# Performance work log

Hardware: AMD Instinct MI355X
Metric: run time of the kernel (lower is better)

The kernel has to match this reference:

```python
import jax, jax.numpy as jnp
import numpy as np

NEG_SLOPE = 0.01
LN_EPS = 1e-5

def _layer_norm(h, g, b):
    mu = jnp.mean(h, axis=-1, keepdims=True)
    var = jnp.mean(jnp.square(h - mu), axis=-1, keepdims=True)
    return (h - mu) * jax.lax.rsqrt(var + LN_EPS) * g + b

def _mlp(h, Wa, ba, g, be, Wb, bb):
    h = h @ Wa + ba
    h = jnp.where(h >= 0, h, NEG_SLOPE * h)  # LeakyReLU
    h = _layer_norm(h, g, be)
    return h @ Wb + bb

def setup_inputs() -> dict:
    N, E = 50000, 800000
    DN, DE, DG, DO = 128, 64, 32, 128
    key = jax.random.key(0)
    ks = jax.random.split(key, 16)
    def lin(k, fan_in, fan_out):
        lim = 1.0 / np.sqrt(fan_in)
        k1, k2 = jax.random.split(k)
        W = jax.random.uniform(k1, (fan_in, fan_out), jnp.float32, -lim, lim)
        b = jax.random.uniform(k2, (fan_out,), jnp.float32, -lim, lim)
        return W, b
    W1a, b1a = lin(ks[0], DN + DE + DG, DO)
    W1b, b1b = lin(ks[1], DO, DO)
    W2a, b2a = lin(ks[2], DN + DO, DO)
    W2b, b2b = lin(ks[3], DO, DO)
    return {
        "x": jax.random.normal(ks[4], (N, DN), jnp.float32),
        "edge_index": jax.random.randint(ks[5], (2, E), 0, N, jnp.int32),
        "edge_attr": jax.random.normal(ks[6], (E, DE), jnp.float32),
        "u": jax.random.normal(ks[7], (DG,), jnp.float32),
        "batch": jnp.zeros((N,), jnp.int32),
        "W1a": W1a, "b1a": b1a,
        "g1": jnp.ones((DO,), jnp.float32), "be1": jnp.zeros((DO,), jnp.float32),
        "W1b": W1b, "b1b": b1b,
        "W2a": W2a, "b2a": b2a,
        "g2": jnp.ones((DO,), jnp.float32), "be2": jnp.zeros((DO,), jnp.float32),
        "W2b": W2b, "b2b": b2b,
    }

def reference(x, edge_index, edge_attr, u, batch,
              W1a, b1a, g1, be1, W1b, b1b,
              W2a, b2a, g2, be2, W2b, b2b):
    src, dest = edge_index[0], edge_index[1]
    E = edge_attr.shape[0]
    N = x.shape[0]
    # gather + concat: [E, DN+DE+DG]
    h = jnp.concatenate([x[src], edge_attr,
                         jnp.broadcast_to(u[None, :], (E, u.shape[0]))], axis=1)
    h = _mlp(h, W1a, b1a, g1, be1, W1b, b1b)
    # scatter_mean by dest
    sums = jax.ops.segment_sum(h, dest, num_segments=N)
    cnt = jax.ops.segment_sum(jnp.ones((E,), h.dtype), dest, num_segments=N)
    agg = sums / jnp.maximum(cnt, 1.0)[:, None]
    return _mlp(jnp.concatenate([x, agg], axis=1), W2a, b2a, g2, be2, W2b, b2b)
```

## Files before the change

kernel.cpp:

```cpp
#include <hip/hip_runtime.h>
#include <hip/hip_fp16.h>
#include <hip/hip_bf16.h>

constexpr int DN = 128, DE = 64, DG = 32, DO = 128;
constexpr float NEG_SLOPE = 0.01f;
constexpr float LN_EPS = 1e-5f;

constexpr int EPB = 128;
constexpr int NB  = 64;
constexpr int T_LD = 136;
constexpr int H_LD = 132;

typedef __attribute__((ext_vector_type(8))) short bf16x8;
typedef __attribute__((ext_vector_type(4))) float f32x4;

__device__ inline unsigned short f2bf(float f) {
    unsigned u = __builtin_bit_cast(unsigned, f);
    u += 0x7FFFu + ((u >> 16) & 1u);
    return (unsigned short)(u >> 16);
}

__device__ inline bf16x8 pk8(float4 p, float4 q) {
    bf16x8 r;
    r[0] = (short)f2bf(p.x); r[1] = (short)f2bf(p.y);
    r[2] = (short)f2bf(p.z); r[3] = (short)f2bf(p.w);
    r[4] = (short)f2bf(q.x); r[5] = (short)f2bf(q.y);
    r[6] = (short)f2bf(q.z); r[7] = (short)f2bf(q.w);
    return r;
}

__global__ void wprep_kernel(const float* __restrict__ W1a,
                             const float* __restrict__ W1b,
                             const float* __restrict__ W2a,
                             const float* __restrict__ W2b,
                             const float* __restrict__ b1a,
                             const float* __restrict__ b1b,
                             const float* __restrict__ u,
                             unsigned short* __restrict__ tab,
                             float* __restrict__ bc,
                             float* __restrict__ b1ap) {
    int idx = blockIdx.x * 256 + threadIdx.x;
    if (idx >= 18 * 512 + 256) return;
    if (idx >= 18 * 512 + 128) {
        int n = idx - (18 * 512 + 128);
        float s = b1a[n];
        for (int k = 0; k < DG; ++k) s += u[k] * W1a[(long)(192 + k) * DO + n];
        b1ap[n] = s;
        return;
    }
    if (idx >= 18 * 512) {
        int n = idx - 18 * 512;
        float s = 0.f;
        for (int j = 0; j < DO; ++j) s += b1b[j] * W2a[(long)(DN + j) * DO + n];
        bc[n] = s;
        return;
    }
    int slabset = idx >> 9;
    int rem = idx & 511;
    int nt = rem >> 6, lane = rem & 63;
    int quad = lane >> 4, l15 = lane & 15;
    int n = nt * 16 + l15;
    union { ushort4 u4[2]; unsigned short s[8]; } o;
    if (slabset < 6) {
        int k0 = slabset * 32 + quad * 8;
#pragma unroll
        for (int j = 0; j < 8; ++j) o.s[j] = f2bf(W1a[(long)(k0 + j) * DO + n]);
    } else if (slabset < 10) {
        int k0 = (slabset - 6) * 32 + quad * 8;
#pragma unroll
        for (int j = 0; j < 8; ++j) o.s[j] = f2bf(W2a[(long)(k0 + j) * DO + n]);
    } else if (slabset < 14) {
        int k0 = (slabset - 10) * 32 + quad * 8;
        float s[8] = {0.f, 0.f, 0.f, 0.f, 0.f, 0.f, 0.f, 0.f};
        for (int j2 = 0; j2 < DO; ++j2) {
            float wa = W2a[(long)(DN + j2) * DO + n];
#pragma unroll
            for (int j = 0; j < 8; ++j) s[j] += W1b[(long)(k0 + j) * DO + j2] * wa;
        }
#pragma unroll
        for (int j = 0; j < 8; ++j) o.s[j] = f2bf(s[j]);
    } else {
        int k0 = (slabset - 14) * 32 + quad * 8;
#pragma unroll
        for (int j = 0; j < 8; ++j) o.s[j] = f2bf(W2b[(long)(k0 + j) * DO + n]);
    }
    *(ushort4*)&tab[(long)idx * 8]     = o.u4[0];
    *(ushort4*)&tab[(long)idx * 8 + 4] = o.u4[1];
}

__global__ void hist_kernel(const int* __restrict__ edge_index,
                            int* __restrict__ counts, int E) {
    int e = blockIdx.x * 256 + threadIdx.x;
    if (e < E) atomicAdd(&counts[edge_index[E + e]], 1);
}

__global__ __launch_bounds__(1024) void scan1_kernel(
    const int* __restrict__ counts, int* __restrict__ offsets,
    int* __restrict__ partials, int N) {
    __shared__ int s_ws[16];
    const int tid = threadIdx.x, lane = tid & 63, wv = tid >> 6;
    int i = blockIdx.x * 1024 + tid;
    int v = (i < N) ? counts[i] : 0;
    int s = v;
#pragma unroll
    for (int off = 1; off < 64; off <<= 1) {
        int t = __shfl_up(s, off, 64);
        if (lane >= off) s += t;
    }
    if (lane == 63) s_ws[wv] = s;
    __syncthreads();
    if (tid < 16) {
        int w = s_ws[tid];
#pragma unroll
        for (int off = 1; off < 16; off <<= 1) {
            int t = __shfl_up(w, off, 16);
            if (tid >= off) w += t;
        }
        s_ws[tid] = w;
    }
    __syncthreads();
    int wbase = wv ? s_ws[wv - 1] : 0;
    if (i < N) offsets[i] = wbase + s - v;
    if (tid == 0) partials[blockIdx.x] = s_ws[15];
}

__global__ void scan2_kernel(int* __restrict__ partials, int P) {
    const int t = threadIdx.x;
    int carry = 0;
    for (int base = 0; base < P; base += 64) {
        int idx = base + t;
        int v = (idx < P) ? partials[idx] : 0;
        int s = v;
#pragma unroll
        for (int off = 1; off < 64; off <<= 1) {
            int w = __shfl_up(s, off, 64);
            if (t >= off) s += w;
        }
        if (idx < P) partials[idx] = carry + s - v;
        carry += __shfl(s, 63, 64);
    }
}

__global__ __launch_bounds__(1024) void scan3_kernel(
    int* __restrict__ offsets, const int* __restrict__ partials,
    int* __restrict__ cursor, int N, int E) {
    int i = blockIdx.x * 1024 + threadIdx.x;
    if (i < N) {
        int o = offsets[i] + partials[blockIdx.x];
        offsets[i] = o; cursor[i] = o;
    }
    if (i == 0) offsets[N] = E;
}

__global__ void scatter_kernel(const int* __restrict__ edge_index,
                               int* __restrict__ cursor,
                               int2* __restrict__ sorted, int E) {
    int e = blockIdx.x * 256 + threadIdx.x;
    if (e < E) {
        int d = edge_index[E + e];
        int pos = atomicAdd(&cursor[d], 1);
        sorted[pos] = make_int2(e, d);
    }
}

__global__ __launch_bounds__(256) void edge_kernel(
    const float* __restrict__ x, const int* __restrict__ edge_index,
    const float* __restrict__ edge_attr,
    const int2* __restrict__ sorted, const unsigned short* __restrict__ tab,
    const float* __restrict__ b1ap, const float* __restrict__ g1,
    const float* __restrict__ be1,
    float* __restrict__ sums, int E)
{
    __shared__ int s_src[EPB], s_eid[EPB], s_dst[EPB];
    __shared__ alignas(16) __half s_h[EPB * H_LD];

    const int tid = threadIdx.x, lane = tid & 63, wave = tid >> 6;
    const int l15 = lane & 15, quad = lane >> 4;
    const int ebase = blockIdx.x * EPB;
    const int evalid = min(EPB, E - ebase);

    if (tid < EPB) {
        bool v = tid < evalid;
        int2 ed = v ? sorted[ebase + tid] : make_int2(0, 0);
        s_eid[tid] = ed.x;
        s_dst[tid] = ed.y;
        s_src[tid] = edge_index[ed.x];
    }
    __syncthreads();

    const int r0 = wave * 32 + l15, r1 = r0 + 16;
    const long xs0 = (long)s_src[r0] * DN;
    const long xs1 = (long)s_src[r1] * DN;
    const long er0 = (long)s_eid[r0] * DE;
    const long er1 = (long)s_eid[r1] * DE;
    const bf16x8* tW1a = (const bf16x8*)tab;
    const int kq = quad * 8;

    f32x4 acc[2][8];
#pragma unroll
    for (int mt = 0; mt < 2; ++mt)
#pragma unroll
        for (int nt = 0; nt < 8; ++nt) acc[mt][nt] = (f32x4){0.f, 0.f, 0.f, 0.f};

#pragma unroll
    for (int ks = 0; ks < 6; ++ks) {
        float4 p0, q0, p1, q1;
        if (ks < 4) {
            const float* b0 = &x[xs0 + ks * 32 + kq];
            const float* b1 = &x[xs1 + ks * 32 + kq];
            p0 = *(const float4*)b0; q0 = *(const float4*)(b0 + 4);
            p1 = *(const float4*)b1; q1 = *(const float4*)(b1 + 4);
        } else {
            int c = ks * 32 - DN + kq;
            const float* b0 = &edge_attr[er0 + c];
            const float* b1 = &edge_attr[er1 + c];
            p0 = *(const float4*)b0; q0 = *(const float4*)(b0 + 4);
            p1 = *(const float4*)b1; q1 = *(const float4*)(b1 + 4);
        }
        bf16x8 a0 = pk8(p0, q0);
        bf16x8 a1 = pk8(p1, q1);
#pragma unroll
        for (int nt = 0; nt < 8; ++nt) {
            bf16x8 b = tW1a[(ks * 8 + nt) * 64 + lane];
            acc[0][nt] = __builtin_amdgcn_mfma_f32_16x16x32_bf16(a0, b, acc[0][nt], 0, 0, 0);
            acc[1][nt] = __builtin_amdgcn_mfma_f32_16x16x32_bf16(a1, b, acc[1][nt], 0, 0, 0);
        }
    }

    float ba[8], gg[8], bb[8];
#pragma unroll
    for (int nt = 0; nt < 8; ++nt) {
        int col = nt * 16 + l15;
        ba[nt] = b1ap[col]; gg[nt] = g1[col]; bb[nt] = be1[col];
    }
#pragma unroll
    for (int mt = 0; mt < 2; ++mt) {
#pragma unroll
        for (int r = 0; r < 4; ++r) {
            float v[8];
            float s = 0.f, q = 0.f;
#pragma unroll
            for (int nt = 0; nt < 8; ++nt) {
                float t = acc[mt][nt][r] + ba[nt];
                t = (t >= 0.f) ? t : NEG_SLOPE * t;
                v[nt] = t; s += t; q += t * t;
            }
#pragma unroll
            for (int off = 1; off < 16; off <<= 1) {
                s += __shfl_xor(s, off, 64);
                q += __shfl_xor(q, off, 64);
            }
            float mu  = s * (1.f / DO);
            float var = q * (1.f / DO) - mu * mu;
            float rs  = rsqrtf(var + LN_EPS);
            int lrow = wave * 32 + mt * 16 + quad * 4 + r;
#pragma unroll
            for (int nt = 0; nt < 8; ++nt) {
                float h  = (v[nt] - mu) * rs * gg[nt] + bb[nt];
                float hp = __shfl_xor(h, 1, 64);
                if ((l15 & 1) == 0) {
                    *(__half2*)&s_h[lrow * H_LD + nt * 16 + l15] =
                        __halves2half2(__float2half_rn(h), __float2half_rn(hp));
                }
            }
        }
    }
    __syncthreads();

    {
        const int d2 = lane * 2;
        int e0 = wave * 32, e1 = min(e0 + 32, evalid);
        if (e0 < e1) {
            float a0 = 0.f, a1 = 0.f;
            int cur = s_dst[e0];
            if (e1 - e0 == 32) {
#pragma unroll
                for (int k = 0; k < 32; ++k) {
                    int e = e0 + k;
                    int dd = s_dst[e];
                    if (dd != cur) {
                        unsafeAtomicAdd(&sums[(long)cur * DO + d2], a0);
                        unsafeAtomicAdd(&sums[(long)cur * DO + d2 + 1], a1);
                        a0 = a1 = 0.f; cur = dd;
                    }
                    float2 hv = __half22float2(*(const __half2*)&s_h[e * H_LD + d2]);
                    a0 += hv.x; a1 += hv.y;
                }
            } else {
                for (int e = e0; e < e1; ++e) {
                    int dd = s_dst[e];
                    if (dd != cur) {
                        unsafeAtomicAdd(&sums[(long)cur * DO + d2], a0);
                        unsafeAtomicAdd(&sums[(long)cur * DO + d2 + 1], a1);
                        a0 = a1 = 0.f; cur = dd;
                    }
                    float2 hv = __half22float2(*(const __half2*)&s_h[e * H_LD + d2]);
                    a0 += hv.x; a1 += hv.y;
                }
            }
            unsafeAtomicAdd(&sums[(long)cur * DO + d2], a0);
            unsafeAtomicAdd(&sums[(long)cur * DO + d2 + 1], a1);
        }
    }
}

__global__ __launch_bounds__(256) void node_kernel(
    const float* __restrict__ x, const float* __restrict__ sums,
    const int* __restrict__ offsets, const unsigned short* __restrict__ tab,
    const float* __restrict__ bc,
    const float* __restrict__ b2a, const float* __restrict__ g2,
    const float* __restrict__ be2, const float* __restrict__ b2b,
    float* __restrict__ out, int N)
{
    __shared__ unsigned short s_t[4][16 * T_LD];

    const int tid = threadIdx.x, lane = tid & 63, wave = tid >> 6;
    const int l15 = lane & 15, quad = lane >> 4;
    const int nbase = blockIdx.x * NB;

    const bf16x8* tW2aT = (const bf16x8*)tab + 6 * 512;
    const bf16x8* tWc   = (const bf16x8*)tab + 10 * 512;
    const bf16x8* tW2b  = (const bf16x8*)tab + 14 * 512;

    const int nodeA = min(nbase + wave * 16 + l15, N - 1);
    const int cntA  = offsets[nodeA + 1] - offsets[nodeA];
    const float invc = 1.f / fmaxf((float)cntA, 1.f);
    const int kq = quad * 8;

    f32x4 acc[8];

#pragma unroll
    for (int nt = 0; nt < 8; ++nt) acc[nt] = (f32x4){0.f, 0.f, 0.f, 0.f};
#pragma unroll
    for (int ks = 0; ks < 8; ++ks) {
        bf16x8 a;
        if (ks < 4) {
            const float* b0 = &x[(long)nodeA * DN + ks * 32 + kq];
            a = pk8(*(const float4*)b0, *(const float4*)(b0 + 4));
        } else {
            const float* sp = &sums[(long)nodeA * DO + (ks - 4) * 32 + kq];
            float4 p = *(const float4*)sp;
            float4 q = *(const float4*)(sp + 4);
            p.x *= invc; p.y *= invc; p.z *= invc; p.w *= invc;
            q.x *= invc; q.y *= invc; q.z *= invc; q.w *= invc;
            a = pk8(p, q);
        }
        const bf16x8* tB = (ks < 4) ? tW2aT : tWc;
        const int kk = (ks < 4) ? ks : ks - 4;
#pragma unroll
        for (int nt = 0; nt < 8; ++nt) {
            bf16x8 b = tB[(kk * 8 + nt) * 64 + lane];
            acc[nt] = __builtin_amdgcn_mfma_f32_16x16x32_bf16(a, b, acc[nt], 0, 0, 0);
        }
    }
    {
        float ba[8], gg[8], bb[8], bcv[8];
#pragma unroll
        for (int nt = 0; nt < 8; ++nt) {
            int col = nt * 16 + l15;
            ba[nt] = b2a[col]; gg[nt] = g2[col]; bb[nt] = be2[col]; bcv[nt] = bc[col];
        }
#pragma unroll
        for (int reg = 0; reg < 4; ++reg) {
            int nodeC = nbase + wave * 16 + quad * 4 + reg;
            int cc = (nodeC < N) ? (offsets[nodeC + 1] - offsets[nodeC]) : 0;
            float cf = (cc > 0) ? 1.f : 0.f;
            float v[8];
            float s = 0.f, q = 0.f;
#pragma unroll
            for (int nt = 0; nt < 8; ++nt) {
                float t = acc[nt][reg] + ba[nt] + cf * bcv[nt];
                t = (t >= 0.f) ? t : NEG_SLOPE * t;
                v[nt] = t; s += t; q += t * t;
            }
#pragma unroll
            for (int off = 1; off < 16; off <<= 1) {
                s += __shfl_xor(s, off, 64);
                q += __shfl_xor(q, off, 64);
            }
            float mu  = s * (1.f / DO);
            float var = q * (1.f / DO) - mu * mu;
            float rs  = rsqrtf(var + LN_EPS);
            int lrow = quad * 4 + reg;
#pragma unroll
            for (int nt = 0; nt < 8; ++nt) {
                float h = (v[nt] - mu) * rs * gg[nt] + bb[nt];
                s_t[wave][lrow * T_LD + nt * 16 + l15] = f2bf(h);
            }
        }
    }

#pragma unroll
    for (int nt = 0; nt < 8; ++nt) acc[nt] = (f32x4){0.f, 0.f, 0.f, 0.f};
#pragma unroll
    for (int ks = 0; ks < 4; ++ks) {
        bf16x8 a = *(const bf16x8*)&s_t[wave][l15 * T_LD + ks * 32 + kq];
#pragma unroll
        for (int nt = 0; nt < 8; ++nt) {
            bf16x8 b = tW2b[(ks * 8 + nt) * 64 + lane];
            acc[nt] = __builtin_amdgcn_mfma_f32_16x16x32_bf16(a, b, acc[nt], 0, 0, 0);
        }
    }
    {
#pragma unroll
        for (int reg = 0; reg < 4; ++reg) {
            int nodeC = nbase + wave * 16 + quad * 4 + reg;
            if (nodeC < N) {
                long base = (long)nodeC * DO;
#pragma unroll
                for (int nt = 0; nt < 8; ++nt)
                    out[base + nt * 16 + l15] = acc[nt][reg] + b2b[nt * 16 + l15];
            }
        }
    }
}

extern "C" void kernel_launch(void* const* d_in, const int* in_sizes, int n_in,
                              void* d_out, int out_size, void* d_ws, size_t ws_size,
                              hipStream_t stream)
{
    const float* x          = (const float*)d_in[0];
    const int*   edge_index = (const int*)d_in[1];
    const float* edge_attr  = (const float*)d_in[2];
    const float* u          = (const float*)d_in[3];
    const float* W1a = (const float*)d_in[5];
    const float* b1a = (const float*)d_in[6];
    const float* g1  = (const float*)d_in[7];
    const float* be1 = (const float*)d_in[8];
    const float* W1b = (const float*)d_in[9];
    const float* b1b = (const float*)d_in[10];
    const float* W2a = (const float*)d_in[11];
    const float* b2a = (const float*)d_in[12];
    const float* g2  = (const float*)d_in[13];
    const float* be2 = (const float*)d_in[14];
    const float* W2b = (const float*)d_in[15];
    const float* b2b = (const float*)d_in[16];

    const int N = in_sizes[0] / DN;
    const int E = in_sizes[2] / DE;
    float* out  = (float*)d_out;

    char* p = (char*)d_ws;
    int2* sorted = (int2*)p;                   p += (size_t)E * sizeof(int2);
    unsigned short* tab = (unsigned short*)p;  p += (size_t)18 * 512 * 8 * sizeof(unsigned short);
    float* bc = (float*)p;                     p += 128 * sizeof(float);
    float* b1ap = (float*)p;                   p += 128 * sizeof(float);
    int* counts = (int*)p;                     p += (size_t)N * sizeof(int);
    int* offsets = (int*)p;                    p += (size_t)(N + 1) * sizeof(int);
    p = (char*)(((uintptr_t)p + 15) & ~(uintptr_t)15);
    int* partials = (int*)p;                   p += 64 * sizeof(int);
    int* cursor = (int*)p;                     p += (size_t)N * sizeof(int);
    float* sums = (float*)d_out;

    (void)hipMemsetAsync(counts, 0, (size_t)N * sizeof(int), stream);
    (void)hipMemsetAsync(d_out, 0, (size_t)N * DO * sizeof(float), stream);

    wprep_kernel<<<(18 * 512 + 256 + 255) / 256, 256, 0, stream>>>(
        W1a, W1b, W2a, W2b, b1a, b1b, u, tab, bc, b1ap);

    const int P = (N + 1023) / 1024;
    hist_kernel<<<(E + 255) / 256, 256, 0, stream>>>(edge_index, counts, E);
    scan1_kernel<<<P, 1024, 0, stream>>>(counts, offsets, partials, N);
    scan2_kernel<<<1, 64, 0, stream>>>(partials, P);
    scan3_kernel<<<P, 1024, 0, stream>>>(offsets, partials, cursor, N, E);
    scatter_kernel<<<(E + 255) / 256, 256, 0, stream>>>(edge_index, cursor, sorted, E);

    const int eblocks = (E + EPB - 1) / EPB;
    edge_kernel<<<eblocks, 256, 0, stream>>>(
        x, edge_index, edge_attr, sorted, tab, b1ap, g1, be1, sums, E);

    const int nblocks = (N + NB - 1) / NB;
    node_kernel<<<nblocks, 256, 0, stream>>>(
        x, sums, offsets, tab, bc, b2a, g2, be2, b2b, out, N);
}
```

Measured before the change: 728.7 us.

## Pre-convert x to bf16, merge scan passes, shrink node blocks, drop edge syncs

Adds a prep kernel that converts x to bf16 once, so the edge kernel's random gathers of source rows move half the bytes and skip per-edge conversion. The second scan pass is folded into the third, which removes one launch. The node kernel now runs one wave per block with 16 nodes. The edge kernel's block-wide barriers are removed by having each wave load only its own edge indices. The cost is an extra full pass over x and a risk of races if any shared data is still read across waves without a barrier.

```diff
diff --git a/kernel.cpp b/kernel.cpp
--- a/kernel.cpp
+++ b/kernel.cpp
@@ -7,7 +7,7 @@
 constexpr float LN_EPS = 1e-5f;
 
 constexpr int EPB = 128;
-constexpr int NB  = 64;
+constexpr int NB  = 16;
 constexpr int T_LD = 136;
 constexpr int H_LD = 132;
 
@@ -88,6 +88,16 @@
     *(ushort4*)&tab[(long)idx * 8 + 4] = o.u4[1];
 }
 
+__global__ void xprep_kernel(const float* __restrict__ x,
+                             unsigned short* __restrict__ xb, int total8) {
+    int i = blockIdx.x * 256 + threadIdx.x;
+    if (i < total8) {
+        const float4* p = (const float4*)x + (long)i * 2;
+        bf16x8 r = pk8(p[0], p[1]);
+        *(bf16x8*)&xb[(long)i * 8] = r;
+    }
+}
+
 __global__ void hist_kernel(const int* __restrict__ edge_index,
                             int* __restrict__ counts, int E) {
     int e = blockIdx.x * 256 + threadIdx.x;
@@ -124,29 +134,25 @@
     if (tid == 0) partials[blockIdx.x] = s_ws[15];
 }
 
-__global__ void scan2_kernel(int* __restrict__ partials, int P) {
-    const int t = threadIdx.x;
-    int carry = 0;
-    for (int base = 0; base < P; base += 64) {
-        int idx = base + t;
-        int v = (idx < P) ? partials[idx] : 0;
-        int s = v;
-#pragma unroll
-        for (int off = 1; off < 64; off <<= 1) {
-            int w = __shfl_up(s, off, 64);
-            if (t >= off) s += w;
-        }
-        if (idx < P) partials[idx] = carry + s - v;
-        carry += __shfl(s, 63, 64);
-    }
-}
-
 __global__ __launch_bounds__(1024) void scan3_kernel(
     int* __restrict__ offsets, const int* __restrict__ partials,
-    int* __restrict__ cursor, int N, int E) {
-    int i = blockIdx.x * 1024 + threadIdx.x;
+    int* __restrict__ cursor, int N, int E, int P) {
+    __shared__ int s_base;
+    const int tid = threadIdx.x;
+    if (tid < 64) {
+        int v = (tid < P) ? partials[tid] : 0;
+        int s = v;
+#pragma unroll
+        for (int off = 1; off < 64; off <<= 1) {
+            int t = __shfl_up(s, off, 64);
+            if (tid >= off) s += t;
+        }
+        if (tid == (int)blockIdx.x) s_base = s - v;
+    }
+    __syncthreads();
+    int i = blockIdx.x * 1024 + tid;
     if (i < N) {
-        int o = offsets[i] + partials[blockIdx.x];
+        int o = offsets[i] + s_base;
         offsets[i] = o; cursor[i] = o;
     }
     if (i == 0) offsets[N] = E;
@@ -164,7 +170,7 @@
 }
 
 __global__ __launch_bounds__(256) void edge_kernel(
-    const float* __restrict__ x, const int* __restrict__ edge_index,
+    const unsigned short* __restrict__ xb, const int* __restrict__ edge_index,
     const float* __restrict__ edge_attr,
     const int2* __restrict__ sorted, const unsigned short* __restrict__ tab,
     const float* __restrict__ b1ap, const float* __restrict__ g1,
@@ -179,14 +185,14 @@
     const int ebase = blockIdx.x * EPB;
     const int evalid = min(EPB, E - ebase);
 
-    if (tid < EPB) {
-        bool v = tid < evalid;
-        int2 ed = v ? sorted[ebase + tid] : make_int2(0, 0);
-        s_eid[tid] = ed.x;
-        s_dst[tid] = ed.y;
-        s_src[tid] = edge_index[ed.x];
-    }
-    __syncthreads();
+    if (lane < 32) {
+        int r = wave * 32 + lane;
+        bool v = r < evalid;
+        int2 ed = v ? sorted[ebase + r] : make_int2(0, 0);
+        s_eid[r] = ed.x;
+        s_dst[r] = ed.y;
+        s_src[r] = edge_index[ed.x];
+    }
 
     const int r0 = wave * 32 + l15, r1 = r0 + 16;
     const long xs0 = (long)s_src[r0] * DN;
@@ -204,21 +210,17 @@
 
 #pragma unroll
     for (int ks = 0; ks < 6; ++ks) {
-        float4 p0, q0, p1, q1;
+        bf16x8 a0, a1;
         if (ks < 4) {
-            const float* b0 = &x[xs0 + ks * 32 + kq];
-            const float* b1 = &x[xs1 + ks * 32 + kq];
-            p0 = *(const float4*)b0; q0 = *(const float4*)(b0 + 4);
-            p1 = *(const float4*)b1; q1 = *(const float4*)(b1 + 4);
+            a0 = *(const bf16x8*)&xb[xs0 + ks * 32 + kq];
+            a1 = *(const bf16x8*)&xb[xs1 + ks * 32 + kq];
         } else {
             int c = ks * 32 - DN + kq;
             const float* b0 = &edge_attr[er0 + c];
             const float* b1 = &edge_attr[er1 + c];
-            p0 = *(const float4*)b0; q0 = *(const float4*)(b0 + 4);
-            p1 = *(const float4*)b1; q1 = *(const float4*)(b1 + 4);
-        }
-        bf16x8 a0 = pk8(p0, q0);
-        bf16x8 a1 = pk8(p1, q1);
+            a0 = pk8(*(const float4*)b0, *(const float4*)(b0 + 4));
+            a1 = pk8(*(const float4*)b1, *(const float4*)(b1 + 4));
+        }
 #pragma unroll
         for (int nt = 0; nt < 8; ++nt) {
             bf16x8 b = tW1a[(ks * 8 + nt) * 64 + lane];
@@ -265,7 +267,6 @@
             }
         }
     }
-    __syncthreads();
 
     {
         const int d2 = lane * 2;
@@ -304,17 +305,17 @@
     }
 }
 
-__global__ __launch_bounds__(256) void node_kernel(
-    const float* __restrict__ x, const float* __restrict__ sums,
+__global__ __launch_bounds__(64) void node_kernel(
+    const unsigned short* __restrict__ xb, const float* __restrict__ sums,
     const int* __restrict__ offsets, const unsigned short* __restrict__ tab,
     const float* __restrict__ bc,
     const float* __restrict__ b2a, const float* __restrict__ g2,
     const float* __restrict__ be2, const float* __restrict__ b2b,
     float* __restrict__ out, int N)
 {
-    __shared__ unsigned short s_t[4][16 * T_LD];
-
-    const int tid = threadIdx.x, lane = tid & 63, wave = tid >> 6;
+    __shared__ unsigned short s_t[16 * T_LD];
+
+    const int lane = threadIdx.x;
     const int l15 = lane & 15, quad = lane >> 4;
     const int nbase = blockIdx.x * NB;
 
@@ -322,7 +323,7 @@
     const bf16x8* tWc   = (const bf16x8*)tab + 10 * 512;
     const bf16x8* tW2b  = (const bf16x8*)tab + 14 * 512;
 
-    const int nodeA = min(nbase + wave * 16 + l15, N - 1);
+    const int nodeA = min(nbase + l15, N - 1);
     const int cntA  = offsets[nodeA + 1] - offsets[nodeA];
     const float invc = 1.f / fmaxf((float)cntA, 1.f);
     const int kq = quad * 8;
@@ -335,8 +336,7 @@
     for (int ks = 0; ks < 8; ++ks) {
         bf16x8 a;
         if (ks < 4) {
-            const float* b0 = &x[(long)nodeA * DN + ks * 32 + kq];
-            a = pk8(*(const float4*)b0, *(const float4*)(b0 + 4));
+            a = *(const bf16x8*)&xb[(long)nodeA * DN + ks * 32 + kq];
         } else {
             const float* sp = &sums[(long)nodeA * DO + (ks - 4) * 32 + kq];
             float4 p = *(const float4*)sp;
@@ -362,7 +362,7 @@
         }
 #pragma unroll
         for (int reg = 0; reg < 4; ++reg) {
-            int nodeC = nbase + wave * 16 + quad * 4 + reg;
+            int nodeC = nbase + quad * 4 + reg;
             int cc = (nodeC < N) ? (offsets[nodeC + 1] - offsets[nodeC]) : 0;
             float cf = (cc > 0) ? 1.f : 0.f;
             float v[8];
@@ -385,7 +385,7 @@
 #pragma unroll
             for (int nt = 0; nt < 8; ++nt) {
                 float h = (v[nt] - mu) * rs * gg[nt] + bb[nt];
-                s_t[wave][lrow * T_LD + nt * 16 + l15] = f2bf(h);
+                s_t[lrow * T_LD + nt * 16 + l15] = f2bf(h);
             }
         }
     }
@@ -394,7 +394,7 @@
     for (int nt = 0; nt < 8; ++nt) acc[nt] = (f32x4){0.f, 0.f, 0.f, 0.f};
 #pragma unroll
     for (int ks = 0; ks < 4; ++ks) {
-        bf16x8 a = *(const bf16x8*)&s_t[wave][l15 * T_LD + ks * 32 + kq];
+        bf16x8 a = *(const bf16x8*)&s_t[l15 * T_LD + ks * 32 + kq];
 #pragma unroll
         for (int nt = 0; nt < 8; ++nt) {
             bf16x8 b = tW2b[(ks * 8 + nt) * 64 + lane];
@@ -404,7 +404,7 @@
     {
 #pragma unroll
         for (int reg = 0; reg < 4; ++reg) {
-            int nodeC = nbase + wave * 16 + quad * 4 + reg;
+            int nodeC = nbase + quad * 4 + reg;
             if (nodeC < N) {
                 long base = (long)nodeC * DO;
 #pragma unroll
@@ -442,6 +442,7 @@
 
     char* p = (char*)d_ws;
     int2* sorted = (int2*)p;                   p += (size_t)E * sizeof(int2);
+    unsigned short* xb = (unsigned short*)p;   p += (size_t)N * DN * sizeof(unsigned short);
     unsigned short* tab = (unsigned short*)p;  p += (size_t)18 * 512 * 8 * sizeof(unsigned short);
     float* bc = (float*)p;                     p += 128 * sizeof(float);
     float* b1ap = (float*)p;                   p += 128 * sizeof(float);
@@ -457,19 +458,19 @@
 
     wprep_kernel<<<(18 * 512 + 256 + 255) / 256, 256, 0, stream>>>(
         W1a, W1b, W2a, W2b, b1a, b1b, u, tab, bc, b1ap);
+    xprep_kernel<<<(N * DN / 8 + 255) / 256, 256, 0, stream>>>(x, xb, N * DN / 8);
 
     const int P = (N + 1023) / 1024;
     hist_kernel<<<(E + 255) / 256, 256, 0, stream>>>(edge_index, counts, E);
     scan1_kernel<<<P, 1024, 0, stream>>>(counts, offsets, partials, N);
-    scan2_kernel<<<1, 64, 0, stream>>>(partials, P);
-    scan3_kernel<<<P, 1024, 0, stream>>>(offsets, partials, cursor, N, E);
+    scan3_kernel<<<P, 1024, 0, stream>>>(offsets, partials, cursor, N, E, P);
     scatter_kernel<<<(E + 255) / 256, 256, 0, stream>>>(edge_index, cursor, sorted, E);
 
     const int eblocks = (E + EPB - 1) / EPB;
     edge_kernel<<<eblocks, 256, 0, stream>>>(
-        x, edge_index, edge_attr, sorted, tab, b1ap, g1, be1, sums, E);
+        xb, edge_index, edge_attr, sorted, tab, b1ap, g1, be1, sums, E);
 
     const int nblocks = (N + NB - 1) / NB;
-    node_kernel<<<nblocks, 256, 0, stream>>>(
-        x, sums, offsets, tab, bc, b2a, g2, be2, b2b, out, N);
-}
+    node_kernel<<<nblocks, 64, 0, stream>>>(
+        xb, sums, offsets, tab, bc, b2a, g2, be2, b2b, out, N);
+}
```

Result: faster. 690.7 us (-5.2%).
